# Performance work log

Hardware: AMD Instinct MI355X
Metric: run time of the kernel (lower is better)

Reference implementation:

```python
import jax, jax.numpy as jnp
import numpy as np

N_NODES = 10000
DEG = 32          # random neighbors per node; +1 self loop (A + I in original)
BATCH = 2
F_IN = 128
D_EMB = 128


def _make_edges():
    # np.where on a dense (A+I) matrix yields edges sorted by source row;
    # we build the same sorted-by-src edge list directly.
    rng = np.random.default_rng(0)
    src = np.repeat(np.arange(N_NODES), DEG + 1)
    dst = rng.integers(0, N_NODES, size=N_NODES * (DEG + 1))
    dst[DEG::DEG + 1] = np.arange(N_NODES)  # guarantee self loops
    return np.stack([src, dst], axis=1).astype(np.int32)  # [E, 2]


def setup_inputs() -> dict:
    key = jax.random.key(0)
    k1, k2, k3 = jax.random.split(key, 3)
    inputs = jax.random.normal(k1, (BATCH, N_NODES, F_IN), jnp.float32)
    W = jax.random.normal(k2, (F_IN, D_EMB), jnp.float32) * 0.1
    W_attn = jax.random.normal(k3, (2 * D_EMB, 1), jnp.float32) * 0.1
    edges = jnp.asarray(_make_edges())
    return {"inputs": inputs, "W": W, "W_attn": W_attn, "edges": edges}


def reference(inputs, W, W_attn, edges):
    # inputs: [B, N, F]; W: [F, D]; W_attn: [2D, 1]; edges: [E, 2] (sorted by src)
    B, N, _ = inputs.shape
    D = W.shape[1]
    src, dst = edges[:, 0], edges[:, 1]

    h = inputs @ W  # [B, N, D] node_states_transformed

    # Original: gather [src,dst] feats, reshape to [B,E,2D], matmul W_attn.
    # Equivalent efficient form: split W_attn and project per node first.
    a_src, a_dst = W_attn[:D, 0], W_attn[D:, 0]
    s = h @ a_src  # [B, N]
    d = h @ a_dst  # [B, N]
    scores = jax.nn.leaky_relu(s[:, src] + d[:, dst], negative_slope=0.2)  # [B, E]
    scores = jnp.exp(jnp.clip(scores, -2.0, 2.0))

    # Faithful to original bug: denominator uses batch 0 only, shared across batch.
    denom = jax.ops.segment_sum(scores[0], src, num_segments=N)  # [N]
    # edges sorted by src => tf.repeat(denom, bincount(src)) == denom[src]
    attn = scores / denom[src][None, :]  # [B, E]

    msgs = h[:, dst] * attn[:, :, None]  # [B, E, D]
    # tf.unsorted_segment_sum with rank-2 segment_ids sums over batch AND edges.
    out = jax.ops.segment_sum(msgs.sum(axis=0), src, num_segments=N)  # [N, D]
    return jnp.broadcast_to(out[None], (B, N, D))
```

## Files before the change

### kernel.cpp

```cpp
#include <hip/hip_runtime.h>
#include <math.h>

#define N_NODES 10000
#define DEG1 33
#define D_EMB 128
#define F_IN 128
#define BATCH 2

typedef short s8v  __attribute__((ext_vector_type(8)));
typedef float f4v  __attribute__((ext_vector_type(4)));

static __device__ __forceinline__ unsigned short f2bf(float f) {
    unsigned int x = __float_as_uint(f);
    unsigned int r = (x + 0x7fffu + ((x >> 16) & 1u)) >> 16;
    return (unsigned short)r;
}
static __device__ __forceinline__ float bf_lo(unsigned int u) { return __uint_as_float(u << 16); }
static __device__ __forceinline__ float bf_hi(unsigned int u) { return __uint_as_float(u & 0xffff0000u); }
static __device__ __forceinline__ float rdlane_f(float v, int l) {
    return __uint_as_float((unsigned int)__builtin_amdgcn_readlane((int)__float_as_uint(v), l));
}

__global__ __launch_bounds__(256) void gat_prep_kernel(
    const float* __restrict__ W, unsigned short* __restrict__ wtf)
{
    const int c = blockIdx.x;
    const int t = threadIdx.x;
    __shared__ float xs[128 * 16];
    #pragma unroll
    for (int r = 0; r < 8; ++r) {
        const int k = r * 16 + (t >> 4);
        const int n = t & 15;
        xs[k * 16 + n] = W[k * 128 + c * 16 + n];
    }
    __syncthreads();
    const int s = t >> 6;
    const int l = t & 63;
    s8v frag;
    #pragma unroll
    for (int j = 0; j < 8; ++j) {
        const int k = s * 32 + (l >> 4) * 8 + j;
        frag[j] = (short)f2bf(xs[k * 16 + (l & 15)]);
    }
    *(s8v*)&wtf[(((size_t)c * 4 + s) * 64 + l) * 8] = frag;
}

__global__ __launch_bounds__(256) void gat_h_kernel(
    const float* __restrict__ X, const unsigned short* __restrict__ wtf,
    const float* __restrict__ Wattn,
    unsigned short* __restrict__ hb, float* __restrict__ s_arr, float* __restrict__ d_arr)
{
    __shared__ float lds_sd[2][2][2][16];
    const int wave = threadIdx.x >> 6;
    const int lane = threadIdx.x & 63;
    const int quad = lane >> 4;
    const int mrow = lane & 15;
    const int rg   = wave >> 1;
    const int half = wave & 1;
    const int row0 = (blockIdx.x * 2 + rg) * 16;

    f4v acc[4];
    #pragma unroll
    for (int cc = 0; cc < 4; ++cc) acc[cc] = (f4v){0.f, 0.f, 0.f, 0.f};

    const float* xrow = X + (size_t)(row0 + mrow) * F_IN;
    #pragma unroll
    for (int s = 0; s < 4; ++s) {
        const int k0 = s * 32 + quad * 8;
        const float4 xa = *(const float4*)&xrow[k0];
        const float4 xbv = *(const float4*)&xrow[k0 + 4];
        s8v a;
        a[0] = (short)f2bf(xa.x);  a[1] = (short)f2bf(xa.y);
        a[2] = (short)f2bf(xa.z);  a[3] = (short)f2bf(xa.w);
        a[4] = (short)f2bf(xbv.x); a[5] = (short)f2bf(xbv.y);
        a[6] = (short)f2bf(xbv.z); a[7] = (short)f2bf(xbv.w);
        #pragma unroll
        for (int cc = 0; cc < 4; ++cc) {
            const int c = half * 4 + cc;
            const s8v b = *(const s8v*)&wtf[(((size_t)c * 4 + s) * 64 + lane) * 8];
            acc[cc] = __builtin_amdgcn_mfma_f32_16x16x32_bf16(a, b, acc[cc], 0, 0, 0);
        }
    }

    const int b = (row0 >= N_NODES) ? 1 : 0;
    #pragma unroll
    for (int r = 0; r < 4; ++r) {
        const int R = row0 + quad * 4 + r;
        const int n = R - b * N_NODES;
        unsigned short* dst = &hb[((size_t)n * 2 + b) * D_EMB + half * 64 + mrow];
        #pragma unroll
        for (int cc = 0; cc < 4; ++cc)
            __builtin_nontemporal_store(f2bf(acc[cc][r]), &dst[cc * 16]);
    }

    float as[4], ad[4];
    #pragma unroll
    for (int cc = 0; cc < 4; ++cc) {
        as[cc] = Wattn[(half * 4 + cc) * 16 + mrow];
        ad[cc] = Wattn[D_EMB + (half * 4 + cc) * 16 + mrow];
    }
    #pragma unroll
    for (int r = 0; r < 4; ++r) {
        float sv = 0.f, dv = 0.f;
        #pragma unroll
        for (int cc = 0; cc < 4; ++cc) {
            sv = fmaf(acc[cc][r], as[cc], sv);
            dv = fmaf(acc[cc][r], ad[cc], dv);
        }
        #pragma unroll
        for (int off = 1; off < 16; off <<= 1) {
            sv += __shfl_xor(sv, off, 16);
            dv += __shfl_xor(dv, off, 16);
        }
        if (mrow == 0) {
            lds_sd[rg][half][0][quad * 4 + r] = sv;
            lds_sd[rg][half][1][quad * 4 + r] = dv;
        }
    }
    __syncthreads();
    const int t = threadIdx.x;
    if (t < 64) {
        const int rg2 = t >> 5, r = (t >> 1) & 15, which = t & 1;
        const float val = lds_sd[rg2][0][which][r] + lds_sd[rg2][1][which][r];
        const int row = (blockIdx.x * 2 + rg2) * 16 + r;
        if (which == 0) s_arr[row] = val; else d_arr[row] = val;
    }
}

__global__ __launch_bounds__(256) void gat_agg_kernel(
    const uint2* __restrict__ h2, const float* __restrict__ s_arr,
    const float* __restrict__ d_arr, const int* __restrict__ edges,
    float* __restrict__ out)
{
    const int i = blockIdx.x * 4 + (threadIdx.x >> 6);
    const int lane = threadIdx.x & 63;

    int dstv = 0; float sc0 = 0.f, sc1 = 0.f;
    if (lane < DEG1) {
        dstv = edges[((size_t)i * DEG1 + lane) * 2 + 1];
        float x0 = s_arr[i] + d_arr[dstv];
        float x1 = s_arr[N_NODES + i] + d_arr[N_NODES + dstv];
        x0 = (x0 >= 0.f) ? x0 : 0.2f * x0;
        x1 = (x1 >= 0.f) ? x1 : 0.2f * x1;
        sc0 = __expf(fminf(fmaxf(x0, -2.f), 2.f));
        sc1 = __expf(fminf(fmaxf(x1, -2.f), 2.f));
    }
    float dsum = sc0;
    #pragma unroll
    for (int off = 1; off < 64; off <<= 1) dsum += __shfl_xor(dsum, off, 64);
    const float inv = 1.f / dsum;
    sc0 *= inv;
    sc1 *= inv;

    float4 acc = make_float4(0.f, 0.f, 0.f, 0.f);
    #pragma unroll
    for (int j = 0; j < DEG1; ++j) {
        const int   dd = __builtin_amdgcn_readlane(dstv, j);
        const float w0 = rdlane_f(sc0, j);
        const float w1 = rdlane_f(sc1, j);
        const float wgt = (lane < 32) ? w0 : w1;
        const uint2 hv = h2[(size_t)dd * 64 + lane];
        acc.x = fmaf(wgt, bf_lo(hv.x), acc.x);
        acc.y = fmaf(wgt, bf_hi(hv.x), acc.y);
        acc.z = fmaf(wgt, bf_lo(hv.y), acc.z);
        acc.w = fmaf(wgt, bf_hi(hv.y), acc.w);
    }
    f4v o;
    o[0] = acc.x + __shfl_xor(acc.x, 32, 64);
    o[1] = acc.y + __shfl_xor(acc.y, 32, 64);
    o[2] = acc.z + __shfl_xor(acc.z, 32, 64);
    o[3] = acc.w + __shfl_xor(acc.w, 32, 64);

    const int b  = lane >> 5;
    const int dl = lane & 31;
    __builtin_nontemporal_store(o, (f4v*)&out[((size_t)b * N_NODES + i) * D_EMB + dl * 4]);
}

extern "C" void kernel_launch(void* const* d_in, const int* in_sizes, int n_in,
                              void* d_out, int out_size, void* d_ws, size_t ws_size,
                              hipStream_t stream) {
    const float* X     = (const float*)d_in[0];
    const float* W     = (const float*)d_in[1];
    const float* Wattn = (const float*)d_in[2];
    const int*   edges = (const int*)d_in[3];
    float* out = (float*)d_out;

    unsigned short* wtf = (unsigned short*)d_ws;
    unsigned short* hb  = wtf + 16384;
    float* s_arr = (float*)(hb + (size_t)BATCH * N_NODES * D_EMB);
    float* d_arr = s_arr + BATCH * N_NODES;

    gat_prep_kernel<<<8, 256, 0, stream>>>(W, wtf);
    gat_h_kernel<<<625, 256, 0, stream>>>(X, wtf, Wattn, hb, s_arr, d_arr);
    gat_agg_kernel<<<N_NODES / 4, 256, 0, stream>>>((const uint2*)hb, s_arr, d_arr, edges, out);
}
```

Baseline: 90.88 us.

## Quantize node features to int8 with per-row scales for gather aggregation

Stores transformed node features as offset int8 with a per-row absmax scale instead of bf16, halving the bytes gathered per neighbor in the aggregation kernel. Attention weights are folded with the row scale and the +128 offset is subtracted after accumulation. The d projection and scales are packed into one float4 per node and s is interleaved by batch for fewer loads. This trades numerical accuracy for bandwidth, and the h kernel now issues byte-sized scattered stores.

```diff
diff --git a/kernel.cpp b/kernel.cpp
--- a/kernel.cpp
+++ b/kernel.cpp
@@ -15,8 +15,6 @@
     unsigned int r = (x + 0x7fffu + ((x >> 16) & 1u)) >> 16;
     return (unsigned short)r;
 }
-static __device__ __forceinline__ float bf_lo(unsigned int u) { return __uint_as_float(u << 16); }
-static __device__ __forceinline__ float bf_hi(unsigned int u) { return __uint_as_float(u & 0xffff0000u); }
 static __device__ __forceinline__ float rdlane_f(float v, int l) {
     return __uint_as_float((unsigned int)__builtin_amdgcn_readlane((int)__float_as_uint(v), l));
 }
@@ -48,9 +46,10 @@
 __global__ __launch_bounds__(256) void gat_h_kernel(
     const float* __restrict__ X, const unsigned short* __restrict__ wtf,
     const float* __restrict__ Wattn,
-    unsigned short* __restrict__ hb, float* __restrict__ s_arr, float* __restrict__ d_arr)
+    unsigned char* __restrict__ hb8, float* __restrict__ pk4, float* __restrict__ s2)
 {
     __shared__ float lds_sd[2][2][2][16];
+    __shared__ float lds_mx[2][2][16];
     const int wave = threadIdx.x >> 6;
     const int lane = threadIdx.x & 63;
     const int quad = lane >> 4;
@@ -82,17 +81,6 @@
         }
     }
 
-    const int b = (row0 >= N_NODES) ? 1 : 0;
-    #pragma unroll
-    for (int r = 0; r < 4; ++r) {
-        const int R = row0 + quad * 4 + r;
-        const int n = R - b * N_NODES;
-        unsigned short* dst = &hb[((size_t)n * 2 + b) * D_EMB + half * 64 + mrow];
-        #pragma unroll
-        for (int cc = 0; cc < 4; ++cc)
-            __builtin_nontemporal_store(f2bf(acc[cc][r]), &dst[cc * 16]);
-    }
-
     float as[4], ad[4];
     #pragma unroll
     for (int cc = 0; cc < 4; ++cc) {
@@ -101,79 +89,113 @@
     }
     #pragma unroll
     for (int r = 0; r < 4; ++r) {
-        float sv = 0.f, dv = 0.f;
+        float sv = 0.f, dv = 0.f, mx = 0.f;
         #pragma unroll
         for (int cc = 0; cc < 4; ++cc) {
             sv = fmaf(acc[cc][r], as[cc], sv);
             dv = fmaf(acc[cc][r], ad[cc], dv);
+            mx = fmaxf(mx, fabsf(acc[cc][r]));
         }
         #pragma unroll
         for (int off = 1; off < 16; off <<= 1) {
             sv += __shfl_xor(sv, off, 16);
             dv += __shfl_xor(dv, off, 16);
+            mx = fmaxf(mx, __shfl_xor(mx, off, 16));
         }
         if (mrow == 0) {
             lds_sd[rg][half][0][quad * 4 + r] = sv;
             lds_sd[rg][half][1][quad * 4 + r] = dv;
+            lds_mx[rg][half][quad * 4 + r] = mx;
         }
     }
     __syncthreads();
+
+    const int b = (row0 >= N_NODES) ? 1 : 0;
+    #pragma unroll
+    for (int r = 0; r < 4; ++r) {
+        const int qr = quad * 4 + r;
+        const float mx = fmaxf(fmaxf(lds_mx[rg][0][qr], lds_mx[rg][1][qr]), 1e-20f);
+        const float inv_s = 127.f / mx;
+        const int n = (row0 + qr) - b * N_NODES;
+        unsigned char* dst = &hb8[((size_t)n * 2 + b) * D_EMB + half * 64 + mrow];
+        #pragma unroll
+        for (int cc = 0; cc < 4; ++cc) {
+            const float tq = fminf(fmaxf(acc[cc][r] * inv_s, -127.f), 127.f);
+            dst[cc * 16] = (unsigned char)(__float2int_rn(tq) + 128);
+        }
+    }
+
     const int t = threadIdx.x;
-    if (t < 64) {
-        const int rg2 = t >> 5, r = (t >> 1) & 15, which = t & 1;
-        const float val = lds_sd[rg2][0][which][r] + lds_sd[rg2][1][which][r];
+    if (t < 32) {
+        const int rg2 = t >> 4, r = t & 15;
         const int row = (blockIdx.x * 2 + rg2) * 16 + r;
-        if (which == 0) s_arr[row] = val; else d_arr[row] = val;
+        const int b2 = (row >= N_NODES) ? 1 : 0;
+        const int n2 = row - b2 * N_NODES;
+        const float s_full = lds_sd[rg2][0][0][r] + lds_sd[rg2][1][0][r];
+        const float d_full = lds_sd[rg2][0][1][r] + lds_sd[rg2][1][1][r];
+        const float mx = fmaxf(fmaxf(lds_mx[rg2][0][r], lds_mx[rg2][1][r]), 1e-20f);
+        s2[(size_t)n2 * 2 + b2] = s_full;
+        pk4[(size_t)n2 * 4 + b2] = d_full;
+        pk4[(size_t)n2 * 4 + 2 + b2] = mx * (1.f / 127.f);
     }
 }
 
 __global__ __launch_bounds__(256) void gat_agg_kernel(
-    const uint2* __restrict__ h2, const float* __restrict__ s_arr,
-    const float* __restrict__ d_arr, const int* __restrict__ edges,
-    float* __restrict__ out)
+    const unsigned int* __restrict__ h4,
+    const float* __restrict__ pk4, const float* __restrict__ s2,
+    const int* __restrict__ edges, float* __restrict__ out)
 {
     const int i = blockIdx.x * 4 + (threadIdx.x >> 6);
     const int lane = threadIdx.x & 63;
 
-    int dstv = 0; float sc0 = 0.f, sc1 = 0.f;
+    int dstv = 0; float sc0 = 0.f, wS0 = 0.f, wS1 = 0.f;
     if (lane < DEG1) {
         dstv = edges[((size_t)i * DEG1 + lane) * 2 + 1];
-        float x0 = s_arr[i] + d_arr[dstv];
-        float x1 = s_arr[N_NODES + i] + d_arr[N_NODES + dstv];
+        const float4 pk = *(const float4*)&pk4[(size_t)dstv * 4];
+        const float s0 = s2[(size_t)i * 2];
+        const float s1 = s2[(size_t)i * 2 + 1];
+        float x0 = s0 + pk.x;
+        float x1 = s1 + pk.y;
         x0 = (x0 >= 0.f) ? x0 : 0.2f * x0;
         x1 = (x1 >= 0.f) ? x1 : 0.2f * x1;
         sc0 = __expf(fminf(fmaxf(x0, -2.f), 2.f));
-        sc1 = __expf(fminf(fmaxf(x1, -2.f), 2.f));
+        const float sc1 = __expf(fminf(fmaxf(x1, -2.f), 2.f));
+        wS0 = sc0 * pk.z;
+        wS1 = sc1 * pk.w;
     }
     float dsum = sc0;
     #pragma unroll
     for (int off = 1; off < 64; off <<= 1) dsum += __shfl_xor(dsum, off, 64);
     const float inv = 1.f / dsum;
-    sc0 *= inv;
-    sc1 *= inv;
+    wS0 *= inv;
+    wS1 *= inv;
+    float csum = wS0 + wS1;
+    #pragma unroll
+    for (int off = 1; off < 64; off <<= 1) csum += __shfl_xor(csum, off, 64);
+    const float C = 128.f * csum;
 
     float4 acc = make_float4(0.f, 0.f, 0.f, 0.f);
     #pragma unroll
     for (int j = 0; j < DEG1; ++j) {
         const int   dd = __builtin_amdgcn_readlane(dstv, j);
-        const float w0 = rdlane_f(sc0, j);
-        const float w1 = rdlane_f(sc1, j);
+        const float w0 = rdlane_f(wS0, j);
+        const float w1 = rdlane_f(wS1, j);
         const float wgt = (lane < 32) ? w0 : w1;
-        const uint2 hv = h2[(size_t)dd * 64 + lane];
-        acc.x = fmaf(wgt, bf_lo(hv.x), acc.x);
-        acc.y = fmaf(wgt, bf_hi(hv.x), acc.y);
-        acc.z = fmaf(wgt, bf_lo(hv.y), acc.z);
-        acc.w = fmaf(wgt, bf_hi(hv.y), acc.w);
-    }
-    f4v o;
-    o[0] = acc.x + __shfl_xor(acc.x, 32, 64);
-    o[1] = acc.y + __shfl_xor(acc.y, 32, 64);
-    o[2] = acc.z + __shfl_xor(acc.z, 32, 64);
-    o[3] = acc.w + __shfl_xor(acc.w, 32, 64);
+        const unsigned int u = h4[(size_t)dd * 64 + lane];
+        acc.x = fmaf(wgt, (float)(u & 0xffu), acc.x);
+        acc.y = fmaf(wgt, (float)((u >> 8) & 0xffu), acc.y);
+        acc.z = fmaf(wgt, (float)((u >> 16) & 0xffu), acc.z);
+        acc.w = fmaf(wgt, (float)(u >> 24), acc.w);
+    }
+    float4 o;
+    o.x = acc.x + __shfl_xor(acc.x, 32, 64) - C;
+    o.y = acc.y + __shfl_xor(acc.y, 32, 64) - C;
+    o.z = acc.z + __shfl_xor(acc.z, 32, 64) - C;
+    o.w = acc.w + __shfl_xor(acc.w, 32, 64) - C;
 
     const int b  = lane >> 5;
     const int dl = lane & 31;
-    __builtin_nontemporal_store(o, (f4v*)&out[((size_t)b * N_NODES + i) * D_EMB + dl * 4]);
+    *(float4*)&out[((size_t)b * N_NODES + i) * D_EMB + dl * 4] = o;
 }
 
 extern "C" void kernel_launch(void* const* d_in, const int* in_sizes, int n_in,
@@ -186,11 +208,11 @@
     float* out = (float*)d_out;
 
     unsigned short* wtf = (unsigned short*)d_ws;
-    unsigned short* hb  = wtf + 16384;
-    float* s_arr = (float*)(hb + (size_t)BATCH * N_NODES * D_EMB);
-    float* d_arr = s_arr + BATCH * N_NODES;
+    unsigned char*  hb8 = (unsigned char*)(wtf + 16384);
+    float* pk4 = (float*)(hb8 + (size_t)BATCH * N_NODES * D_EMB);
+    float* s2  = pk4 + (size_t)N_NODES * 4;
 
     gat_prep_kernel<<<8, 256, 0, stream>>>(W, wtf);
-    gat_h_kernel<<<625, 256, 0, stream>>>(X, wtf, Wattn, hb, s_arr, d_arr);
-    gat_agg_kernel<<<N_NODES / 4, 256, 0, stream>>>((const uint2*)hb, s_arr, d_arr, edges, out);
-}
+    gat_h_kernel<<<625, 256, 0, stream>>>(X, wtf, Wattn, hb8, pk4, s2);
+    gat_agg_kernel<<<N_NODES / 4, 256, 0, stream>>>((const unsigned int*)hb8, pk4, s2, edges, out);
+}
```

Result: faster. 86.38 us (-5.0%).
